# Kernel tuning notes

Hardware: AMD Instinct MI355X
Metric: run time of the kernel (lower is better)

## Reference

```python
import jax, jax.numpy as jnp
import numpy as np

S, B, H, K = 4096, 1, 2048, 2  # seq_len, batch (forced to 1 by the view()), hidden_dim, conv kernel
EMBED = K * K                  # embed_dim must equal kernel_size**2
THRESHOLD = 0.0


def setup_inputs() -> dict:
    key = jax.random.key(0)
    k0, k1, k2 = jax.random.split(key, 3)
    inputs = jax.random.normal(k0, (S, B, EMBED), dtype=jnp.float32)
    # ConvFilter params: Conv2d(1,1,K) on a KxK patch == dot with flattened kernel + bias
    conv_w = jax.random.normal(k1, (EMBED,), dtype=jnp.float32) * 0.5
    conv_b = jnp.zeros((1,), dtype=jnp.float32)
    # Four gate Linears (1+H -> H) stacked column-wise into one (1+H, 4H) matmul
    # order: forget | input | update | output  (same math as 4 separate nn.Linear)
    w_gates = (jax.random.normal(k2, (1 + H, 4 * H), dtype=jnp.float32)
               / np.sqrt(1.0 + H)).astype(jnp.float32)
    b_gates = jnp.zeros((4 * H,), dtype=jnp.float32)
    return {"inputs": inputs, "conv_w": conv_w, "conv_b": conv_b,
            "w_gates": w_gates, "b_gates": b_gates}


def reference(inputs, conv_w, conv_b, w_gates, b_gates):
    S_, B_, _ = inputs.shape
    H_ = w_gates.shape[1] // 4

    # Conv preprocess (vectorized over all timesteps): each (K,K) token patch
    # -> scalar sigmoid(conv(x) - threshold), then mean over the per-step batch
    # (batch==1, so the mean is the value itself, matching torch's .mean()).
    conv_scalar = jax.nn.sigmoid(inputs @ conv_w + conv_b[0] - THRESHOLD)  # (S, B)
    conv_scalar = jnp.mean(conv_scalar, axis=1, keepdims=True)             # (S, 1)
    conv_out = jnp.broadcast_to(conv_scalar[:, :, None], (S_, B_, 1))      # (S, B, 1)

    hx0 = jnp.zeros((B_, H_), dtype=inputs.dtype)
    cx0 = jnp.zeros((B_, H_), dtype=inputs.dtype)

    def step(carry, c_t):
        hx, cx = carry
        combined = jnp.concatenate([c_t, hx], axis=1)        # (B, 1+H)
        gates = combined @ w_gates + b_gates                  # (B, 4H) fused 4-gate GEMM
        f, i, g, o = jnp.split(gates, 4, axis=1)
        f = jax.nn.sigmoid(f)
        i = jax.nn.sigmoid(i)
        g = jnp.tanh(g)
        o = jax.nn.sigmoid(o)
        cx = f * cx + i * g
        hx = o * jnp.tanh(cx)
        return (hx, cx), hx

    (hx, cx), stacked = jax.lax.scan(step, (hx0, cx0), conv_out)
    return stacked, hx, cx
```

## Files before the change

kernel.cpp:

```cpp
#include <hip/hip_runtime.h>
#include <math.h>

#define S_LEN 4096
#define HID   2048
#define NBLK  256
#define NTHR  512

typedef unsigned long long u64;


__global__ __launch_bounds__(NTHR, 2)
void qlstm_persistent(const float* __restrict__ inp,
                      const float* __restrict__ conv_w,
                      const float* __restrict__ conv_b,
                      const float* __restrict__ Wg,
                      const float* __restrict__ bg,
                      float* __restrict__ out,
                      float* __restrict__ ws)
{
    const int b   = blockIdx.x;
    const int tid = threadIdx.x;
    const int l   = tid & 63;
    const int wv  = tid >> 6;

    u64* tb0 = (u64*)ws;
    u64* tb1 = tb0 + HID + 16;

    __shared__ __align__(16) float hx_lds[HID];
    __shared__ __align__(16) float conv_lds[S_LEN];
    __shared__ float gates_lds[32];
    __shared__ float colw0[32];
    __shared__ float colb[32];

    {
        const float cw0 = conv_w[0], cw1 = conv_w[1], cw2 = conv_w[2], cw3 = conv_w[3];
        const float cb  = conv_b[0];
        for (int g = tid; g < S_LEN; g += NTHR) {
            float4 x = ((const float4*)inp)[g];
            float v = x.x*cw0 + x.y*cw1 + x.z*cw2 + x.w*cw3 + cb;
            conv_lds[g] = 1.0f / (1.0f + expf(-v));
        }
    }

    int jcol[4];
    #pragma unroll
    for (int c = 0; c < 4; ++c) {
        int cgi  = 4*wv + c;
        int gate = cgi >> 3;
        int mi   = cgi & 7;
        jcol[c]  = (gate << 11) + (b * 8 + mi);
    }
    if (l == 0) {
        #pragma unroll
        for (int c = 0; c < 4; ++c) {
            int cgi = 4*wv + c;
            colw0[cgi] = Wg[jcol[c]];
            colb[cgi]  = bg[jcol[c]];
        }
    }

    float wreg[4][32];
    #pragma unroll
    for (int j = 0; j < 8; ++j)
        #pragma unroll
        for (int r = 0; r < 4; ++r) {
            const float* rowp = Wg + (size_t)(1 + 4*l + 256*j + r) * 8192;
            #pragma unroll
            for (int c = 0; c < 4; ++c)
                wreg[c][4*j + r] = rowp[jcol[c]];
        }

    float cx = 0.0f;
    const int m_out = b * 8 + tid;

    if (tid < 8)
        __hip_atomic_store(&tb0[m_out], (u64)1 << 32,
                           __ATOMIC_RELAXED, __HIP_MEMORY_SCOPE_AGENT);

    const int ebase = (wv << 8) + l;

    for (int t = 0; t < S_LEN; ++t) {
        const unsigned want = (unsigned)(t + 1);
        u64* tb = (t & 1) ? tb1 : tb0;
        u64* tn = (t & 1) ? tb0 : tb1;

        u64 v0 = 0, v1 = 0, v2 = 0, v3 = 0;
        unsigned pend = 0xFu;
        do {
            if (pend & 1u) v0 = __hip_atomic_load(&tb[ebase      ], __ATOMIC_RELAXED, __HIP_MEMORY_SCOPE_AGENT);
            if (pend & 2u) v1 = __hip_atomic_load(&tb[ebase +  64], __ATOMIC_RELAXED, __HIP_MEMORY_SCOPE_AGENT);
            if (pend & 4u) v2 = __hip_atomic_load(&tb[ebase + 128], __ATOMIC_RELAXED, __HIP_MEMORY_SCOPE_AGENT);
            if (pend & 8u) v3 = __hip_atomic_load(&tb[ebase + 192], __ATOMIC_RELAXED, __HIP_MEMORY_SCOPE_AGENT);
            if ((unsigned)(v0 >> 32) == want) pend &= ~1u;
            if ((unsigned)(v1 >> 32) == want) pend &= ~2u;
            if ((unsigned)(v2 >> 32) == want) pend &= ~4u;
            if ((unsigned)(v3 >> 32) == want) pend &= ~8u;
        } while (pend);
        hx_lds[ebase      ] = __uint_as_float((unsigned)v0);
        hx_lds[ebase +  64] = __uint_as_float((unsigned)v1);
        hx_lds[ebase + 128] = __uint_as_float((unsigned)v2);
        hx_lds[ebase + 192] = __uint_as_float((unsigned)v3);
        __syncthreads();

        const float4* hl = (const float4*)hx_lds;
        float acc0 = 0.f, acc1 = 0.f, acc2 = 0.f, acc3 = 0.f;
        #pragma unroll
        for (int j = 0; j < 8; ++j) {
            float4 h = hl[l + 64*j];
            acc0 = fmaf(h.x, wreg[0][4*j+0], acc0);
            acc1 = fmaf(h.x, wreg[1][4*j+0], acc1);
            acc2 = fmaf(h.x, wreg[2][4*j+0], acc2);
            acc3 = fmaf(h.x, wreg[3][4*j+0], acc3);
            acc0 = fmaf(h.y, wreg[0][4*j+1], acc0);
            acc1 = fmaf(h.y, wreg[1][4*j+1], acc1);
            acc2 = fmaf(h.y, wreg[2][4*j+1], acc2);
            acc3 = fmaf(h.y, wreg[3][4*j+1], acc3);
            acc0 = fmaf(h.z, wreg[0][4*j+2], acc0);
            acc1 = fmaf(h.z, wreg[1][4*j+2], acc1);
            acc2 = fmaf(h.z, wreg[2][4*j+2], acc2);
            acc3 = fmaf(h.z, wreg[3][4*j+2], acc3);
            acc0 = fmaf(h.w, wreg[0][4*j+3], acc0);
            acc1 = fmaf(h.w, wreg[1][4*j+3], acc1);
            acc2 = fmaf(h.w, wreg[2][4*j+3], acc2);
            acc3 = fmaf(h.w, wreg[3][4*j+3], acc3);
        }
        #pragma unroll
        for (int off = 32; off; off >>= 1) {
            acc0 += __shfl_down(acc0, off, 64);
            acc1 += __shfl_down(acc1, off, 64);
            acc2 += __shfl_down(acc2, off, 64);
            acc3 += __shfl_down(acc3, off, 64);
        }
        if (l == 0) {
            gates_lds[4*wv + 0] = acc0;
            gates_lds[4*wv + 1] = acc1;
            gates_lds[4*wv + 2] = acc2;
            gates_lds[4*wv + 3] = acc3;
        }
        __syncthreads();

        if (tid < 8) {
            float ct = conv_lds[t];
            float fg = gates_lds[tid]      + ct*colw0[tid]      + colb[tid];
            float ig = gates_lds[8 + tid]  + ct*colw0[8 + tid]  + colb[8 + tid];
            float gg = gates_lds[16 + tid] + ct*colw0[16 + tid] + colb[16 + tid];
            float og = gates_lds[24 + tid] + ct*colw0[24 + tid] + colb[24 + tid];
            float f  = 1.0f / (1.0f + expf(-fg));
            float ii = 1.0f / (1.0f + expf(-ig));
            float gv = tanhf(gg);
            float o  = 1.0f / (1.0f + expf(-og));
            cx = f * cx + ii * gv;
            float hx = o * tanhf(cx);
            __hip_atomic_store(&tn[m_out],
                               ((u64)(unsigned)(t + 2) << 32) | (u64)__float_as_uint(hx),
                               __ATOMIC_RELAXED, __HIP_MEMORY_SCOPE_AGENT);
            out[(size_t)t * HID + m_out] = hx;
            if (t == S_LEN - 1) {
                out[(size_t)S_LEN * HID + m_out]       = hx;
                out[(size_t)S_LEN * HID + HID + m_out] = cx;
            }
        }
    }
}

extern "C" void kernel_launch(void* const* d_in, const int* in_sizes, int n_in,
                              void* d_out, int out_size, void* d_ws, size_t ws_size,
                              hipStream_t stream) {
    const float* inp    = (const float*)d_in[0];
    const float* conv_w = (const float*)d_in[1];
    const float* conv_b = (const float*)d_in[2];
    const float* Wg     = (const float*)d_in[3];
    const float* bg     = (const float*)d_in[4];
    float* out = (float*)d_out;
    float* ws  = (float*)d_ws;


    void* args[] = {(void*)&inp, (void*)&conv_w, (void*)&conv_b,
                    (void*)&Wg, (void*)&bg, (void*)&out, (void*)&ws};
    hipLaunchCooperativeKernel((void*)qlstm_persistent,
                               dim3(NBLK), dim3(NTHR), args, 0, stream);
}
```

Before: 11.65 ms.

## Pack hx and step tag into 32-bit words, one hidden unit per wave

Each wavefront now computes all four gates of one hidden unit, so the gate values are combined with wave shuffles. This removes the gates_lds staging, the second block barrier and the single-lane serial tail. The hx exchange shrinks from 64-bit (tag, value) pairs to 32-bit words, with a 2-bit step tag stored in the low mantissa bits. The next step's flags are prefetched before the dot product so polling overlaps compute. Packed v2f FMAs and exp2/rcp-based sigmoid and tanh replace the libm calls. In exchange hx loses 2 mantissa bits and the activations are less precise. The 2-bit tag scheme also risks matching stale or zero-initialised workspace values: the tag expected on the first prefetch is 0, so zero-filled flags would pass as ready.

Result: slower. 27.52 ms (+136.3%).

```diff
diff --git a/kernel.cpp b/kernel.cpp
--- a/kernel.cpp
+++ b/kernel.cpp
@@ -6,8 +6,15 @@
 #define NBLK  256
 #define NTHR  512
 
+typedef unsigned int       u32;
 typedef unsigned long long u64;
+typedef float v2f __attribute__((ext_vector_type(2)));
 
+
+__device__ __forceinline__ float fast_sigmoid(float x) {
+    float e = __builtin_amdgcn_exp2f(-1.44269504f * x);
+    return __builtin_amdgcn_rcpf(1.0f + e);
+}
 
 __global__ __launch_bounds__(NTHR, 2)
 void qlstm_persistent(const float* __restrict__ inp,
@@ -23,14 +30,11 @@
     const int l   = tid & 63;
     const int wv  = tid >> 6;
 
-    u64* tb0 = (u64*)ws;
-    u64* tb1 = tb0 + HID + 16;
+    u32* tb0 = (u32*)ws;
+    u32* tb1 = tb0 + HID + 32;
 
     __shared__ __align__(16) float hx_lds[HID];
     __shared__ __align__(16) float conv_lds[S_LEN];
-    __shared__ float gates_lds[32];
-    __shared__ float colw0[32];
-    __shared__ float colb[32];
 
     {
         const float cw0 = conv_w[0], cw1 = conv_w[1], cw2 = conv_w[2], cw3 = conv_w[3];
@@ -38,127 +42,134 @@
         for (int g = tid; g < S_LEN; g += NTHR) {
             float4 x = ((const float4*)inp)[g];
             float v = x.x*cw0 + x.y*cw1 + x.z*cw2 + x.w*cw3 + cb;
-            conv_lds[g] = 1.0f / (1.0f + expf(-v));
+            conv_lds[g] = fast_sigmoid(v);
+        }
+    }
+    ((float4*)hx_lds)[tid] = make_float4(0.f, 0.f, 0.f, 0.f);
+
+    const int m = b * 8 + wv;
+
+    float w0 = 0.f, bb = 0.f;
+    if (l < 4) {
+        int jc = (l << 11) + m;
+        w0 = Wg[jc];
+        bb = bg[jc];
+    }
+
+    v2f wA[4][8], wB[4][8];
+    #pragma unroll
+    for (int j = 0; j < 8; ++j) {
+        #pragma unroll
+        for (int c = 0; c < 4; ++c) {
+            const int jc = (c << 11) + m;
+            const float* r0 = Wg + (size_t)(1 + 4*l + 256*j + 0) * 8192 + jc;
+            const float* r1 = Wg + (size_t)(1 + 4*l + 256*j + 1) * 8192 + jc;
+            const float* r2 = Wg + (size_t)(1 + 4*l + 256*j + 2) * 8192 + jc;
+            const float* r3 = Wg + (size_t)(1 + 4*l + 256*j + 3) * 8192 + jc;
+            v2f a; a.x = *r0; a.y = *r1;
+            v2f bvec; bvec.x = *r2; bvec.y = *r3;
+            wA[c][j] = a;
+            wB[c][j] = bvec;
         }
     }
 
-    int jcol[4];
-    #pragma unroll
-    for (int c = 0; c < 4; ++c) {
-        int cgi  = 4*wv + c;
-        int gate = cgi >> 3;
-        int mi   = cgi & 7;
-        jcol[c]  = (gate << 11) + (b * 8 + mi);
-    }
-    if (l == 0) {
-        #pragma unroll
-        for (int c = 0; c < 4; ++c) {
-            int cgi = 4*wv + c;
-            colw0[cgi] = Wg[jcol[c]];
-            colb[cgi]  = bg[jcol[c]];
-        }
-    }
+    float cx = 0.0f;
+    const int e0 = tid * 4;
+    u32 v0 = 0, v1 = 0, v2 = 0, v3 = 0;
+    unsigned pend = 0;
 
-    float wreg[4][32];
-    #pragma unroll
-    for (int j = 0; j < 8; ++j)
-        #pragma unroll
-        for (int r = 0; r < 4; ++r) {
-            const float* rowp = Wg + (size_t)(1 + 4*l + 256*j + r) * 8192;
-            #pragma unroll
-            for (int c = 0; c < 4; ++c)
-                wreg[c][4*j + r] = rowp[jcol[c]];
-        }
-
-    float cx = 0.0f;
-    const int m_out = b * 8 + tid;
-
-    if (tid < 8)
-        __hip_atomic_store(&tb0[m_out], (u64)1 << 32,
-                           __ATOMIC_RELAXED, __HIP_MEMORY_SCOPE_AGENT);
-
-    const int ebase = (wv << 8) + l;
+    __syncthreads();
 
     for (int t = 0; t < S_LEN; ++t) {
-        const unsigned want = (unsigned)(t + 1);
-        u64* tb = (t & 1) ? tb1 : tb0;
-        u64* tn = (t & 1) ? tb0 : tb1;
+        u32* tb = (t & 1) ? tb1 : tb0;
+        u32* tn = (t & 1) ? tb0 : tb1;
 
-        u64 v0 = 0, v1 = 0, v2 = 0, v3 = 0;
-        unsigned pend = 0xFu;
-        do {
-            if (pend & 1u) v0 = __hip_atomic_load(&tb[ebase      ], __ATOMIC_RELAXED, __HIP_MEMORY_SCOPE_AGENT);
-            if (pend & 2u) v1 = __hip_atomic_load(&tb[ebase +  64], __ATOMIC_RELAXED, __HIP_MEMORY_SCOPE_AGENT);
-            if (pend & 4u) v2 = __hip_atomic_load(&tb[ebase + 128], __ATOMIC_RELAXED, __HIP_MEMORY_SCOPE_AGENT);
-            if (pend & 8u) v3 = __hip_atomic_load(&tb[ebase + 192], __ATOMIC_RELAXED, __HIP_MEMORY_SCOPE_AGENT);
-            if ((unsigned)(v0 >> 32) == want) pend &= ~1u;
-            if ((unsigned)(v1 >> 32) == want) pend &= ~2u;
-            if ((unsigned)(v2 >> 32) == want) pend &= ~4u;
-            if ((unsigned)(v3 >> 32) == want) pend &= ~8u;
-        } while (pend);
-        hx_lds[ebase      ] = __uint_as_float((unsigned)v0);
-        hx_lds[ebase +  64] = __uint_as_float((unsigned)v1);
-        hx_lds[ebase + 128] = __uint_as_float((unsigned)v2);
-        hx_lds[ebase + 192] = __uint_as_float((unsigned)v3);
-        __syncthreads();
-
-        const float4* hl = (const float4*)hx_lds;
-        float acc0 = 0.f, acc1 = 0.f, acc2 = 0.f, acc3 = 0.f;
-        #pragma unroll
-        for (int j = 0; j < 8; ++j) {
-            float4 h = hl[l + 64*j];
-            acc0 = fmaf(h.x, wreg[0][4*j+0], acc0);
-            acc1 = fmaf(h.x, wreg[1][4*j+0], acc1);
-            acc2 = fmaf(h.x, wreg[2][4*j+0], acc2);
-            acc3 = fmaf(h.x, wreg[3][4*j+0], acc3);
-            acc0 = fmaf(h.y, wreg[0][4*j+1], acc0);
-            acc1 = fmaf(h.y, wreg[1][4*j+1], acc1);
-            acc2 = fmaf(h.y, wreg[2][4*j+1], acc2);
-            acc3 = fmaf(h.y, wreg[3][4*j+1], acc3);
-            acc0 = fmaf(h.z, wreg[0][4*j+2], acc0);
-            acc1 = fmaf(h.z, wreg[1][4*j+2], acc1);
-            acc2 = fmaf(h.z, wreg[2][4*j+2], acc2);
-            acc3 = fmaf(h.z, wreg[3][4*j+2], acc3);
-            acc0 = fmaf(h.w, wreg[0][4*j+3], acc0);
-            acc1 = fmaf(h.w, wreg[1][4*j+3], acc1);
-            acc2 = fmaf(h.w, wreg[2][4*j+3], acc2);
-            acc3 = fmaf(h.w, wreg[3][4*j+3], acc3);
+        const u32 want = (u32)(((t + 1) & 3) ^ 2);
+        while (pend) {
+            u32 a0 = 0, a1 = 0, a2 = 0, a3 = 0;
+            if (pend & 1u) a0 = __hip_atomic_load(&tb[e0 + 0], __ATOMIC_RELAXED, __HIP_MEMORY_SCOPE_AGENT);
+            if (pend & 2u) a1 = __hip_atomic_load(&tb[e0 + 1], __ATOMIC_RELAXED, __HIP_MEMORY_SCOPE_AGENT);
+            if (pend & 4u) a2 = __hip_atomic_load(&tb[e0 + 2], __ATOMIC_RELAXED, __HIP_MEMORY_SCOPE_AGENT);
+            if (pend & 8u) a3 = __hip_atomic_load(&tb[e0 + 3], __ATOMIC_RELAXED, __HIP_MEMORY_SCOPE_AGENT);
+            if ((pend & 1u) && (a0 & 3u) == want) { v0 = a0; pend &= ~1u; }
+            if ((pend & 2u) && (a1 & 3u) == want) { v1 = a1; pend &= ~2u; }
+            if ((pend & 4u) && (a2 & 3u) == want) { v2 = a2; pend &= ~4u; }
+            if ((pend & 8u) && (a3 & 3u) == want) { v3 = a3; pend &= ~8u; }
         }
-        #pragma unroll
-        for (int off = 32; off; off >>= 1) {
-            acc0 += __shfl_down(acc0, off, 64);
-            acc1 += __shfl_down(acc1, off, 64);
-            acc2 += __shfl_down(acc2, off, 64);
-            acc3 += __shfl_down(acc3, off, 64);
-        }
-        if (l == 0) {
-            gates_lds[4*wv + 0] = acc0;
-            gates_lds[4*wv + 1] = acc1;
-            gates_lds[4*wv + 2] = acc2;
-            gates_lds[4*wv + 3] = acc3;
+        if (t) {
+            uint4 st;
+            st.x = v0 & ~3u; st.y = v1 & ~3u; st.z = v2 & ~3u; st.w = v3 & ~3u;
+            ((uint4*)hx_lds)[tid] = st;
         }
         __syncthreads();
 
-        if (tid < 8) {
-            float ct = conv_lds[t];
-            float fg = gates_lds[tid]      + ct*colw0[tid]      + colb[tid];
-            float ig = gates_lds[8 + tid]  + ct*colw0[8 + tid]  + colb[8 + tid];
-            float gg = gates_lds[16 + tid] + ct*colw0[16 + tid] + colb[16 + tid];
-            float og = gates_lds[24 + tid] + ct*colw0[24 + tid] + colb[24 + tid];
-            float f  = 1.0f / (1.0f + expf(-fg));
-            float ii = 1.0f / (1.0f + expf(-ig));
-            float gv = tanhf(gg);
-            float o  = 1.0f / (1.0f + expf(-og));
-            cx = f * cx + ii * gv;
-            float hx = o * tanhf(cx);
-            __hip_atomic_store(&tn[m_out],
-                               ((u64)(unsigned)(t + 2) << 32) | (u64)__float_as_uint(hx),
-                               __ATOMIC_RELAXED, __HIP_MEMORY_SCOPE_AGENT);
-            out[(size_t)t * HID + m_out] = hx;
+        u64 qa = 0, qb = 0;
+        if (t + 1 < S_LEN) {
+            qa = __hip_atomic_load((const u64*)&tn[e0],     __ATOMIC_RELAXED, __HIP_MEMORY_SCOPE_AGENT);
+            qb = __hip_atomic_load((const u64*)&tn[e0 + 2], __ATOMIC_RELAXED, __HIP_MEMORY_SCOPE_AGENT);
+        }
+
+        const v2f* hl2 = (const v2f*)hx_lds;
+        v2f acc0, acc1, acc2, acc3;
+        acc0 = 0.f; acc1 = 0.f; acc2 = 0.f; acc3 = 0.f;
+        #pragma unroll
+        for (int j = 0; j < 8; ++j) {
+            v2f hA = hl2[2*(l + 64*j)];
+            v2f hB = hl2[2*(l + 64*j) + 1];
+            acc0 += hA * wA[0][j];  acc0 += hB * wB[0][j];
+            acc1 += hA * wA[1][j];  acc1 += hB * wB[1][j];
+            acc2 += hA * wA[2][j];  acc2 += hB * wB[2][j];
+            acc3 += hA * wA[3][j];  acc3 += hB * wB[3][j];
+        }
+        float s0 = acc0.x + acc0.y;
+        float s1 = acc1.x + acc1.y;
+        float s2 = acc2.x + acc2.y;
+        float s3 = acc3.x + acc3.y;
+        #pragma unroll
+        for (int off = 1; off < 64; off <<= 1) {
+            s0 += __shfl_xor(s0, off, 64);
+            s1 += __shfl_xor(s1, off, 64);
+            s2 += __shfl_xor(s2, off, 64);
+            s3 += __shfl_xor(s3, off, 64);
+        }
+
+        float a = s0;
+        a = (l == 1) ? s1 : a;
+        a = (l == 2) ? s2 : a;
+        a = (l == 3) ? s3 : a;
+        float ct = conv_lds[t];
+        float x  = a + ct * w0 + bb;
+        float xs = (l == 2) ? 2.0f * x : x;
+        float y  = fast_sigmoid(xs);
+        float g  = (l == 2) ? 2.0f * y - 1.0f : y;
+
+        float f  = __shfl(g, 0, 64);
+        float ii = __shfl(g, 1, 64);
+        float gg = __shfl(g, 2, 64);
+        float o  = __shfl(g, 3, 64);
+        cx = f * cx + ii * gg;
+        float th = 2.0f * fast_sigmoid(2.0f * cx) - 1.0f;
+        float hx = o * th;
+
+        if (l == 0) {
+            u32 word = (__float_as_uint(hx) & ~3u) | (u32)(((t + 2) & 3) ^ 2);
+            __hip_atomic_store(&tn[m], word, __ATOMIC_RELAXED, __HIP_MEMORY_SCOPE_AGENT);
+            out[(size_t)t * HID + m] = hx;
             if (t == S_LEN - 1) {
-                out[(size_t)S_LEN * HID + m_out]       = hx;
-                out[(size_t)S_LEN * HID + HID + m_out] = cx;
+                out[(size_t)S_LEN * HID + m]       = hx;
+                out[(size_t)S_LEN * HID + HID + m] = cx;
             }
+        }
+
+        if (t + 1 < S_LEN) {
+            const u32 wn = (u32)(((t + 2) & 3) ^ 2);
+            u32 c0 = (u32)qa, c1 = (u32)(qa >> 32);
+            u32 c2 = (u32)qb, c3 = (u32)(qb >> 32);
+            pend = 0xFu;
+            if ((c0 & 3u) == wn) { v0 = c0; pend &= ~1u; }
+            if ((c1 & 3u) == wn) { v1 = c1; pend &= ~2u; }
+            if ((c2 & 3u) == wn) { v2 = c2; pend &= ~4u; }
+            if ((c3 & 3u) == wn) { v3 = c3; pend &= ~8u; }
         }
     }
 }
@@ -174,7 +185,6 @@
     float* out = (float*)d_out;
     float* ws  = (float*)d_ws;
 
-
     void* args[] = {(void*)&inp, (void*)&conv_w, (void*)&conv_b,
                     (void*)&Wg, (void*)&bg, (void*)&out, (void*)&ws};
     hipLaunchCooperativeKernel((void*)qlstm_persistent,
```

## Pack LSTM hidden-state flags into low mantissa bits and use fast transcendentals

Applied to the files above, without the earlier changes.

Replaces the 64-bit (value, step-counter) exchange words with 32-bit words that carry a 2-bit step tag in the low mantissa bits of hx. Each thread now polls four contiguous entries with two 64-bit loads and stores them to LDS as one uint4, which halves exchange traffic and cuts the polling load count. Step 0 is skipped by zero-initialising LDS, polling backs off with s_sleep, and the gate wave gets raised priority. Sigmoid and tanh use exp2/rcp intrinsics. The trade-off is precision: the two truncated hx mantissa bits and the approximate math may shift numerics.

Measured after the change: 13.46 ms. 1.16x slower.

```diff
diff --git a/kernel.cpp b/kernel.cpp
--- a/kernel.cpp
+++ b/kernel.cpp
@@ -6,8 +6,14 @@
 #define NBLK  256
 #define NTHR  512
 
+typedef unsigned int       u32;
 typedef unsigned long long u64;
 
+
+__device__ __forceinline__ float fast_sigmoid(float x) {
+    float e = __builtin_amdgcn_exp2f(-1.44269504f * x);
+    return __builtin_amdgcn_rcpf(1.0f + e);
+}
 
 __global__ __launch_bounds__(NTHR, 2)
 void qlstm_persistent(const float* __restrict__ inp,
@@ -23,8 +29,8 @@
     const int l   = tid & 63;
     const int wv  = tid >> 6;
 
-    u64* tb0 = (u64*)ws;
-    u64* tb1 = tb0 + HID + 16;
+    u32* tb0 = (u32*)ws;
+    u32* tb1 = tb0 + HID + 16;
 
     __shared__ __align__(16) float hx_lds[HID];
     __shared__ __align__(16) float conv_lds[S_LEN];
@@ -38,9 +44,10 @@
         for (int g = tid; g < S_LEN; g += NTHR) {
             float4 x = ((const float4*)inp)[g];
             float v = x.x*cw0 + x.y*cw1 + x.z*cw2 + x.w*cw3 + cb;
-            conv_lds[g] = 1.0f / (1.0f + expf(-v));
+            conv_lds[g] = fast_sigmoid(v);
         }
     }
+    ((float4*)hx_lds)[tid] = make_float4(0.f, 0.f, 0.f, 0.f);
 
     int jcol[4];
     #pragma unroll
@@ -69,37 +76,43 @@
             for (int c = 0; c < 4; ++c)
                 wreg[c][4*j + r] = rowp[jcol[c]];
         }
+    asm volatile("" ::: "memory");
 
     float cx = 0.0f;
     const int m_out = b * 8 + tid;
+    const int e0 = tid * 4;
 
-    if (tid < 8)
-        __hip_atomic_store(&tb0[m_out], (u64)1 << 32,
-                           __ATOMIC_RELAXED, __HIP_MEMORY_SCOPE_AGENT);
-
-    const int ebase = (wv << 8) + l;
+    u32 v0 = 0, v1 = 0, v2 = 0, v3 = 0;
+    unsigned pend = 0;
 
     for (int t = 0; t < S_LEN; ++t) {
-        const unsigned want = (unsigned)(t + 1);
-        u64* tb = (t & 1) ? tb1 : tb0;
-        u64* tn = (t & 1) ? tb0 : tb1;
+        u32* tb = (t & 1) ? tb1 : tb0;
+        u32* tn = (t & 1) ? tb0 : tb1;
 
-        u64 v0 = 0, v1 = 0, v2 = 0, v3 = 0;
-        unsigned pend = 0xFu;
-        do {
-            if (pend & 1u) v0 = __hip_atomic_load(&tb[ebase      ], __ATOMIC_RELAXED, __HIP_MEMORY_SCOPE_AGENT);
-            if (pend & 2u) v1 = __hip_atomic_load(&tb[ebase +  64], __ATOMIC_RELAXED, __HIP_MEMORY_SCOPE_AGENT);
-            if (pend & 4u) v2 = __hip_atomic_load(&tb[ebase + 128], __ATOMIC_RELAXED, __HIP_MEMORY_SCOPE_AGENT);
-            if (pend & 8u) v3 = __hip_atomic_load(&tb[ebase + 192], __ATOMIC_RELAXED, __HIP_MEMORY_SCOPE_AGENT);
-            if ((unsigned)(v0 >> 32) == want) pend &= ~1u;
-            if ((unsigned)(v1 >> 32) == want) pend &= ~2u;
-            if ((unsigned)(v2 >> 32) == want) pend &= ~4u;
-            if ((unsigned)(v3 >> 32) == want) pend &= ~8u;
-        } while (pend);
-        hx_lds[ebase      ] = __uint_as_float((unsigned)v0);
-        hx_lds[ebase +  64] = __uint_as_float((unsigned)v1);
-        hx_lds[ebase + 128] = __uint_as_float((unsigned)v2);
-        hx_lds[ebase + 192] = __uint_as_float((unsigned)v3);
+        if (pend) {
+            const u32 want = ((u32)(t + 1) & 3u) ^ 2u;
+            int slept = 0;
+            do {
+                if (slept) __builtin_amdgcn_s_sleep(1);
+                slept = 1;
+                u64 qa = 0, qb = 0;
+                if (pend & 3u)
+                    qa = __hip_atomic_load((const u64*)(tb + e0),
+                                           __ATOMIC_RELAXED, __HIP_MEMORY_SCOPE_AGENT);
+                if (pend & 12u)
+                    qb = __hip_atomic_load((const u64*)(tb + e0 + 2),
+                                           __ATOMIC_RELAXED, __HIP_MEMORY_SCOPE_AGENT);
+                u32 c0 = (u32)qa, c1 = (u32)(qa >> 32);
+                u32 c2 = (u32)qb, c3 = (u32)(qb >> 32);
+                if ((pend & 1u) && (c0 & 3u) == want) { v0 = c0; pend &= ~1u; }
+                if ((pend & 2u) && (c1 & 3u) == want) { v1 = c1; pend &= ~2u; }
+                if ((pend & 4u) && (c2 & 3u) == want) { v2 = c2; pend &= ~4u; }
+                if ((pend & 8u) && (c3 & 3u) == want) { v3 = c3; pend &= ~8u; }
+            } while (pend);
+            uint4 st;
+            st.x = v0 & ~3u; st.y = v1 & ~3u; st.z = v2 & ~3u; st.w = v3 & ~3u;
+            ((uint4*)hx_lds)[tid] = st;
+        }
         __syncthreads();
 
         const float4* hl = (const float4*)hx_lds;
@@ -139,20 +152,21 @@
         }
         __syncthreads();
 
+        if (wv == 0) __builtin_amdgcn_s_setprio(1);
         if (tid < 8) {
             float ct = conv_lds[t];
             float fg = gates_lds[tid]      + ct*colw0[tid]      + colb[tid];
             float ig = gates_lds[8 + tid]  + ct*colw0[8 + tid]  + colb[8 + tid];
             float gg = gates_lds[16 + tid] + ct*colw0[16 + tid] + colb[16 + tid];
             float og = gates_lds[24 + tid] + ct*colw0[24 + tid] + colb[24 + tid];
-            float f  = 1.0f / (1.0f + expf(-fg));
-            float ii = 1.0f / (1.0f + expf(-ig));
-            float gv = tanhf(gg);
-            float o  = 1.0f / (1.0f + expf(-og));
+            float f  = fast_sigmoid(fg);
+            float ii = fast_sigmoid(ig);
+            float gv = 2.0f * fast_sigmoid(2.0f * gg) - 1.0f;
+            float o  = fast_sigmoid(og);
             cx = f * cx + ii * gv;
-            float hx = o * tanhf(cx);
-            __hip_atomic_store(&tn[m_out],
-                               ((u64)(unsigned)(t + 2) << 32) | (u64)__float_as_uint(hx),
+            float hx = o * (2.0f * fast_sigmoid(2.0f * cx) - 1.0f);
+            u32 word = (__float_as_uint(hx) & ~3u) | (((u32)(t + 2) & 3u) ^ 2u);
+            __hip_atomic_store(&tn[m_out], word,
                                __ATOMIC_RELAXED, __HIP_MEMORY_SCOPE_AGENT);
             out[(size_t)t * HID + m_out] = hx;
             if (t == S_LEN - 1) {
@@ -160,6 +174,9 @@
                 out[(size_t)S_LEN * HID + HID + m_out] = cx;
             }
         }
+        if (wv == 0) __builtin_amdgcn_s_setprio(0);
+
+        pend = 0xFu;
     }
 }
 
@@ -174,7 +191,6 @@
     float* out = (float*)d_out;
     float* ws  = (float*)d_ws;
 
-
     void* args[] = {(void*)&inp, (void*)&conv_w, (void*)&conv_b,
                     (void*)&Wg, (void*)&bg, (void*)&out, (void*)&ws};
     hipLaunchCooperativeKernel((void*)qlstm_persistent,
```
